# Optimization experiments

Measured on AMD Instinct MI355X. Metric: run time of the kernel, lower is better.

## Reference

```python
import jax, jax.numpy as jnp
import numpy as np

T = 8192  # context/question length (input_shape[2])
D = 128   # feature dim (input_shape[3])


def setup_inputs() -> dict:
    key = jax.random.key(0)
    k1, k2 = jax.random.split(key)
    x = jax.random.normal(k1, (2, 1, T, D), dtype=jnp.float32)
    kernel = jax.random.normal(k2, (3 * D,), dtype=jnp.float32)
    return {"x": x, "kernel": kernel}


def reference(x, kernel):
    context = x[0, 0]   # (T, D)
    question = x[1, 0]  # (T, D)
    w_c, w_q, w_m = kernel[:D], kernel[D:2 * D], kernel[2 * D:]

    # Additive similarity: S[i,j] = c_i.w_c + q_j.w_q + (c_i*q_j).w_m
    # Avoids materializing the (T, T, 3D) tiled/concatenated tensor.
    S = (context @ w_c)[:, None] + (question @ w_q)[None, :] \
        + (context * w_m) @ question.T  # (T, T)

    A = jax.nn.softmax(S, axis=-1)  # row-wise softmax, as tf.nn.softmax on 2D

    # C2Q attention: U_A[i] = sum_j A[i,j] * q_j
    U_A = A @ question  # (T, D)

    # Q2C attention: b = row-max of A, h = sum_i b_i * c_i, tiled over rows
    b = jnp.max(A, axis=1)          # (T,)
    h = b @ context                 # (D,)
    H_A = jnp.broadcast_to(h, (T, D))

    # megamerge: [c, U_A, c*U_A, c*H_A]
    G = jnp.concatenate([context, U_A, context * U_A, context * H_A], axis=-1)
    return G  # (T, 4D)
```

## Files before the change

kernel.cpp:

```cpp
#include <hip/hip_runtime.h>
#include <hip/hip_bf16.h>

#define T 8192
#define D 128
#define NSPLIT 8
#define JLEN (T / NSPLIT)
#define BN 64
#define NITER (JLEN / BN)
#define BM 128
#define LOG2E 1.44269504088896f

typedef _Float16 half2_t __attribute__((ext_vector_type(2)));
typedef _Float16 half4_t __attribute__((ext_vector_type(4)));
typedef _Float16 half8_t __attribute__((ext_vector_type(8)));
typedef __fp16 fp16x2_t __attribute__((ext_vector_type(2)));
typedef float floatx4 __attribute__((ext_vector_type(4)));
typedef float floatx16 __attribute__((ext_vector_type(16)));

__global__ void prep_kernel(const float* __restrict__ x, const float* __restrict__ kern,
                            _Float16* __restrict__ q16, _Float16* __restrict__ qT16,
                            _Float16* __restrict__ cm16, float* __restrict__ qq2) {
    const float* context  = x;
    const float* question = x + (size_t)T * D;
    const float* wq = kern + D;
    const float* wm = kern + 2 * D;
    __shared__ __align__(16) _Float16 tile[32][136];
    int j0 = blockIdx.x * 32;
    int t = threadIdx.x;
    int c4 = t & 31;
    int rsub = t >> 5;
    float4 wqv = ((const float4*)wq)[c4];
    float4 wmv = ((const float4*)wm)[c4];
    for (int p = 0; p < 4; ++p) {
        int row = p * 8 + rsub;
        float4 q = ((const float4*)(question + (size_t)(j0 + row) * D))[c4];
        float4 c = ((const float4*)(context  + (size_t)(j0 + row) * D))[c4];
        half4_t qh;
        qh[0] = (_Float16)q.x; qh[1] = (_Float16)q.y; qh[2] = (_Float16)q.z; qh[3] = (_Float16)q.w;
        *(half4_t*)(q16 + (size_t)(j0 + row) * D + c4 * 4) = qh;
        *(half4_t*)&tile[row][c4 * 4] = qh;
        half4_t ch;
        ch[0] = (_Float16)(c.x * wmv.x * LOG2E); ch[1] = (_Float16)(c.y * wmv.y * LOG2E);
        ch[2] = (_Float16)(c.z * wmv.z * LOG2E); ch[3] = (_Float16)(c.w * wmv.w * LOG2E);
        *(half4_t*)(cm16 + (size_t)(j0 + row) * D + c4 * 4) = ch;
        float s = q.x * wqv.x + q.y * wqv.y + q.z * wqv.z + q.w * wqv.w;
        for (int dx = 1; dx <= 16; dx <<= 1) s += __shfl_xor(s, dx);
        if (c4 == 0) qq2[j0 + row] = s * LOG2E;
    }
    __syncthreads();
    for (int p = 0; p < 2; ++p) {
        int chunk = t + p * 256;
        int d = chunk >> 2, jo = (chunk & 3) * 8;
        half8_t v;
        for (int s2 = 0; s2 < 8; ++s2) v[s2] = tile[jo + s2][d];
        *(half8_t*)(qT16 + (size_t)d * T + j0 + jo) = v;
    }
}

__global__ __launch_bounds__(256, 2)
void flash_kernel(const _Float16* __restrict__ q16, const _Float16* __restrict__ qT16,
                  const _Float16* __restrict__ cm16, const float* __restrict__ qq2,
                  unsigned char* __restrict__ Opart, float* __restrict__ mpart,
                  float* __restrict__ lpart) {
    __shared__ __align__(16) _Float16 Kt[2][64][136];
    __shared__ __align__(16) _Float16 Vt[2][128][64];
    __shared__ __align__(16) float qqs[JLEN];

    const int bx = blockIdx.x;
    const int rb = bx >> 3;
    const int sp = bx & 7;
    const int tid = threadIdx.x;
    const int wave = tid >> 6;
    const int lane = tid & 63;
    const int l31 = lane & 31;
    const int h = lane >> 5;
    const int rbase = rb * BM + wave * 32;
    const int q = rbase + l31;
    const int sig = (l31 & 19) | ((l31 & 4) << 1) | ((l31 & 8) >> 1);

    ((float4*)qqs)[tid] = ((const float4*)(qq2 + (size_t)sp * JLEN))[tid];

    half8_t qfrag[8];
#pragma unroll
    for (int ks = 0; ks < 8; ++ks)
        qfrag[ks] = *(const half8_t*)(cm16 + (size_t)q * D + ks * 16 + h * 8);

    floatx16 acc[4];
#pragma unroll
    for (int nt = 0; nt < 4; ++nt)
#pragma unroll
        for (int r = 0; r < 16; ++r) acc[nt][r] = 0.f;
    float m_run = -INFINITY, l_run = 0.f;

    const int j0 = sp * JLEN;
    half8_t kreg[4], vreg[4];
#pragma unroll
    for (int k = 0; k < 4; ++k) {
        int idx = tid + k * 256;
        kreg[k] = *(const half8_t*)(q16 + (size_t)(j0 + (idx >> 4)) * D + (idx & 15) * 8);
        vreg[k] = *(const half8_t*)(qT16 + (size_t)(idx >> 3) * T + j0 + (idx & 7) * 8);
    }
#pragma unroll
    for (int k = 0; k < 4; ++k) {
        int idx = tid + k * 256;
        *(half8_t*)&Kt[0][idx >> 4][(idx & 15) * 8] = kreg[k];
        int dr = idx >> 3, c8 = idx & 7;
        *(half8_t*)&Vt[0][dr][((c8 + (dr & 7)) & 7) * 8] = vreg[k];
    }
#pragma unroll
    for (int k = 0; k < 4; ++k) {
        int idx = tid + k * 256;
        kreg[k] = *(const half8_t*)(q16 + (size_t)(j0 + BN + (idx >> 4)) * D + (idx & 15) * 8);
        vreg[k] = *(const half8_t*)(qT16 + (size_t)(idx >> 3) * T + j0 + BN + (idx & 7) * 8);
    }
    __syncthreads();

    for (int it = 0; it < NITER; ++it) {
        const int cur = it & 1;
        if (it + 1 < NITER) {
#pragma unroll
            for (int k = 0; k < 4; ++k) {
                int idx = tid + k * 256;
                *(half8_t*)&Kt[cur ^ 1][idx >> 4][(idx & 15) * 8] = kreg[k];
                int dr = idx >> 3, c8 = idx & 7;
                *(half8_t*)&Vt[cur ^ 1][dr][((c8 + (dr & 7)) & 7) * 8] = vreg[k];
            }
        }
        if (it + 2 < NITER) {
            int jn = j0 + (it + 2) * BN;
#pragma unroll
            for (int k = 0; k < 4; ++k) {
                int idx = tid + k * 256;
                kreg[k] = *(const half8_t*)(q16 + (size_t)(jn + (idx >> 4)) * D + (idx & 15) * 8);
                vreg[k] = *(const half8_t*)(qT16 + (size_t)(idx >> 3) * T + jn + (idx & 7) * 8);
            }
        }

        floatx16 St[2];
#pragma unroll
        for (int jt = 0; jt < 2; ++jt) {
            const float* qb = &qqs[it * 64 + jt * 32];
            float4 b0 = *(const float4*)(qb + 8 * h);
            float4 b1 = *(const float4*)(qb + 4 + 8 * h);
            float4 b2 = *(const float4*)(qb + 16 + 8 * h);
            float4 b3 = *(const float4*)(qb + 20 + 8 * h);
            St[jt][0]  = b0.x; St[jt][1]  = b0.y; St[jt][2]  = b0.z; St[jt][3]  = b0.w;
            St[jt][4]  = b1.x; St[jt][5]  = b1.y; St[jt][6]  = b1.z; St[jt][7]  = b1.w;
            St[jt][8]  = b2.x; St[jt][9]  = b2.y; St[jt][10] = b2.z; St[jt][11] = b2.w;
            St[jt][12] = b3.x; St[jt][13] = b3.y; St[jt][14] = b3.z; St[jt][15] = b3.w;
            __builtin_amdgcn_s_setprio(1);
#pragma unroll
            for (int ks = 0; ks < 8; ++ks) {
                half8_t a = *(const half8_t*)&Kt[cur][jt * 32 + sig][ks * 16 + h * 8];
                St[jt] = __builtin_amdgcn_mfma_f32_32x32x16_f16(a, qfrag[ks], St[jt], 0, 0, 0);
            }
            __builtin_amdgcn_s_setprio(0);
        }

        float mx = St[0][0];
#pragma unroll
        for (int r = 1; r < 16; ++r) mx = fmaxf(mx, St[0][r]);
#pragma unroll
        for (int r = 0; r < 16; ++r) mx = fmaxf(mx, St[1][r]);
        mx = fmaxf(mx, __shfl_xor(mx, 32));
        if (__any(mx > m_run)) {
            float mnew = fmaxf(m_run, mx);
            float alpha = __builtin_amdgcn_exp2f(m_run - mnew);
#pragma unroll
            for (int nt = 0; nt < 4; ++nt)
#pragma unroll
                for (int r = 0; r < 16; ++r) acc[nt][r] *= alpha;
            l_run *= alpha;
            m_run = mnew;
        }
        half2_t pp[2][8];
        float ps = 0.f;
#pragma unroll
        for (int jt = 0; jt < 2; ++jt)
#pragma unroll
            for (int r2 = 0; r2 < 8; ++r2) {
                float p0 = __builtin_amdgcn_exp2f(St[jt][2 * r2]     - m_run);
                float p1 = __builtin_amdgcn_exp2f(St[jt][2 * r2 + 1] - m_run);
                ps += p0 + p1;
                fp16x2_t pk = __builtin_amdgcn_cvt_pkrtz(p0, p1);
                pp[jt][r2] = __builtin_bit_cast(half2_t, pk);
            }
        ps += __shfl_xor(ps, 32);
        l_run += ps;

        __builtin_amdgcn_s_setprio(1);
#pragma unroll
        for (int jt = 0; jt < 2; ++jt)
#pragma unroll
            for (int kb = 0; kb < 2; ++kb) {
                half8_t pb;
                pb[0] = pp[jt][kb * 4 + 0][0]; pb[1] = pp[jt][kb * 4 + 0][1];
                pb[2] = pp[jt][kb * 4 + 1][0]; pb[3] = pp[jt][kb * 4 + 1][1];
                pb[4] = pp[jt][kb * 4 + 2][0]; pb[5] = pp[jt][kb * 4 + 2][1];
                pb[6] = pp[jt][kb * 4 + 3][0]; pb[7] = pp[jt][kb * 4 + 3][1];
                const int pg = ((jt * 4 + kb * 2 + h) + (l31 & 7)) & 7;
#pragma unroll
                for (int nt = 0; nt < 4; ++nt) {
                    half8_t va = *(const half8_t*)&Vt[cur][nt * 32 + l31][pg * 8];
                    acc[nt] = __builtin_amdgcn_mfma_f32_32x32x16_f16(va, pb, acc[nt], 0, 0, 0);
                }
            }
        __builtin_amdgcn_s_setprio(0);
        __syncthreads();
    }

    if (h == 0) {
        mpart[(size_t)sp * T + q] = m_run;
        lpart[(size_t)sp * T + q] = l_run;
    }
    float rinv = 1.0f / l_run;
#pragma unroll
    for (int nt = 0; nt < 4; ++nt)
#pragma unroll
        for (int rg = 0; rg < 4; ++rg) {
            float v0 = acc[nt][rg * 4 + 0] * rinv;
            float v1 = acc[nt][rg * 4 + 1] * rinv;
            float v2 = acc[nt][rg * 4 + 2] * rinv;
            float v3 = acc[nt][rg * 4 + 3] * rinv;
            unsigned u = (unsigned)__builtin_amdgcn_cvt_pk_fp8_f32(v0, v1, 0, false);
            u = (unsigned)__builtin_amdgcn_cvt_pk_fp8_f32(v2, v3, u, true);
            *(unsigned*)(Opart + ((size_t)sp * T + q) * D + nt * 32 + rg * 8 + 4 * h) = u;
        }
}

__global__ void combine_kernel(const float* __restrict__ x, const float* __restrict__ mpart,
                               const float* __restrict__ lpart, float* __restrict__ hpart) {
    __shared__ float linv_s[128];
    int b = blockIdx.x, t = threadIdx.x;
    if (t < 128) {
        int i = b * 128 + t;
        float mp[NSPLIT];
        float mstar = -INFINITY;
        for (int sp2 = 0; sp2 < NSPLIT; ++sp2) {
            mp[sp2] = mpart[(size_t)sp2 * T + i];
            mstar = fmaxf(mstar, mp[sp2]);
        }
        float L = 0.f;
        for (int sp2 = 0; sp2 < NSPLIT; ++sp2)
            L += __builtin_amdgcn_exp2f(mp[sp2] - mstar) * lpart[(size_t)sp2 * T + i];
        linv_s[t] = 1.0f / L;
    }
    __syncthreads();
    int d = t & 127, g = t >> 7;
    int r0 = g * 64;
    float s = 0.f;
    for (int r = 0; r < 64; ++r)
        s += x[(size_t)(b * 128 + r0 + r) * D + d] * linv_s[r0 + r];
    hpart[(size_t)(b * 2 + g) * 128 + d] = s;
}

__global__ void merge_kernel(const unsigned char* __restrict__ Opart, const float* __restrict__ mpart,
                             const float* __restrict__ lpart, float* __restrict__ U_A,
                             const float* __restrict__ hpart, float* __restrict__ h) {
    int t = threadIdx.x;
    if (blockIdx.x == 0 && t < 128) {
        float s = 0.f;
        for (int k = 0; k < 128; ++k) s += hpart[(size_t)k * 128 + t];
        h[t] = s;
    }
    int i = blockIdx.x * 16 + (t >> 4);
    int c = t & 15;
    float mp[NSPLIT];
    float mstar = -INFINITY;
    for (int sp = 0; sp < NSPLIT; ++sp) {
        mp[sp] = mpart[(size_t)sp * T + i];
        mstar = fmaxf(mstar, mp[sp]);
    }
    float L = 0.f;
    float u[8];
    for (int k = 0; k < 8; ++k) u[k] = 0.f;
    int d0 = c * 8;
    for (int sp = 0; sp < NSPLIT; ++sp) {
        float w = __builtin_amdgcn_exp2f(mp[sp] - mstar) * lpart[(size_t)sp * T + i];
        L += w;
        uint2 ow = *(const uint2*)(Opart + ((size_t)sp * T + i) * D + d0);
        u[0] += __builtin_amdgcn_cvt_f32_fp8(ow.x, 0) * w;
        u[1] += __builtin_amdgcn_cvt_f32_fp8(ow.x, 1) * w;
        u[2] += __builtin_amdgcn_cvt_f32_fp8(ow.x, 2) * w;
        u[3] += __builtin_amdgcn_cvt_f32_fp8(ow.x, 3) * w;
        u[4] += __builtin_amdgcn_cvt_f32_fp8(ow.y, 0) * w;
        u[5] += __builtin_amdgcn_cvt_f32_fp8(ow.y, 1) * w;
        u[6] += __builtin_amdgcn_cvt_f32_fp8(ow.y, 2) * w;
        u[7] += __builtin_amdgcn_cvt_f32_fp8(ow.y, 3) * w;
    }
    float invL = 1.0f / L;
    float4 s0 = make_float4(u[0] * invL, u[1] * invL, u[2] * invL, u[3] * invL);
    float4 s1 = make_float4(u[4] * invL, u[5] * invL, u[6] * invL, u[7] * invL);
    *(float4*)(U_A + (size_t)i * D + d0) = s0;
    *(float4*)(U_A + (size_t)i * D + d0 + 4) = s1;
}

__global__ void assemble_kernel(const float* __restrict__ x, const float* __restrict__ U_A,
                                const float* __restrict__ h, float* __restrict__ out) {
    const float* context = x;
    int gid = blockIdx.x * 256 + threadIdx.x;
    int base = gid * 4;
    int i = base >> 9;
    int c = base & 511;
    int seg = c >> 7, d = c & 127;
    float4 r;
    if (seg == 0) {
        r = *(const float4*)(context + (size_t)i * D + d);
    } else if (seg == 1) {
        r = *(const float4*)(U_A + (size_t)i * D + d);
    } else if (seg == 2) {
        float4 a = *(const float4*)(context + (size_t)i * D + d);
        float4 b = *(const float4*)(U_A + (size_t)i * D + d);
        r = make_float4(a.x * b.x, a.y * b.y, a.z * b.z, a.w * b.w);
    } else {
        float4 a = *(const float4*)(context + (size_t)i * D + d);
        float4 b = *(const float4*)(h + d);
        r = make_float4(a.x * b.x, a.y * b.y, a.z * b.z, a.w * b.w);
    }
    *(float4*)(out + base) = r;
}

extern "C" void kernel_launch(void* const* d_in, const int* in_sizes, int n_in,
                              void* d_out, int out_size, void* d_ws, size_t ws_size,
                              hipStream_t stream) {
    const float* x = (const float*)d_in[0];
    const float* kern = (const float*)d_in[1];
    float* out = (float*)d_out;

    char* w = (char*)d_ws;
    size_t off = 0;
    _Float16* q16  = (_Float16*)(w + off); off += (size_t)T * D * 2;
    _Float16* qT16 = (_Float16*)(w + off); off += (size_t)T * D * 2;
    _Float16* cm16 = (_Float16*)(w + off); off += (size_t)T * D * 2;
    float* qq2   = (float*)(w + off); off += (size_t)T * 4;
    float* mpart = (float*)(w + off); off += (size_t)NSPLIT * T * 4;
    float* lpart = (float*)(w + off); off += (size_t)NSPLIT * T * 4;
    float* U_A   = (float*)(w + off); off += (size_t)T * D * 4;
    float* hpart = (float*)(w + off); off += (size_t)128 * 128 * 4;
    float* h     = (float*)(w + off); off += (size_t)D * 4;

    unsigned char* Opart = (unsigned char*)d_out;

    prep_kernel<<<256, 256, 0, stream>>>(x, kern, q16, qT16, cm16, qq2);
    flash_kernel<<<512, 256, 0, stream>>>(q16, qT16, cm16, qq2, Opart, mpart, lpart);
    combine_kernel<<<64, 256, 0, stream>>>(x, mpart, lpart, hpart);
    merge_kernel<<<512, 256, 0, stream>>>(Opart, mpart, lpart, U_A, hpart, h);
    assemble_kernel<<<4096, 256, 0, stream>>>(x, U_A, h, out);
}
```

Measured before the change: 127.9 us.

## Software-pipeline QK MFMA one tile ahead and fuse combine/merge into one launch

The flash kernel now computes the score tile for the next iteration while running the softmax and PV MMA for the current one. It also splits the K and V shared-memory stores around a mid-loop barrier that replaces the end-of-loop one, and uses tree reductions for the row max and partial sums. The combine and merge kernels become a single tail kernel whose extra blocks accumulate h with atomicAdd, with h zeroed in the prep kernel, which saves one launch and the hpart reduction. The cost is more live registers for the second score tile, which can lower occupancy, and float atomic ordering makes h nondeterministic.

```diff
diff --git a/kernel.cpp b/kernel.cpp
--- a/kernel.cpp
+++ b/kernel.cpp
@@ -19,7 +19,8 @@
 
 __global__ void prep_kernel(const float* __restrict__ x, const float* __restrict__ kern,
                             _Float16* __restrict__ q16, _Float16* __restrict__ qT16,
-                            _Float16* __restrict__ cm16, float* __restrict__ qq2) {
+                            _Float16* __restrict__ cm16, float* __restrict__ qq2,
+                            float* __restrict__ h) {
     const float* context  = x;
     const float* question = x + (size_t)T * D;
     const float* wq = kern + D;
@@ -27,6 +28,7 @@
     __shared__ __align__(16) _Float16 tile[32][136];
     int j0 = blockIdx.x * 32;
     int t = threadIdx.x;
+    if (blockIdx.x == 0 && t < 128) h[t] = 0.f;
     int c4 = t & 31;
     int rsub = t >> 5;
     float4 wqv = ((const float4*)wq)[c4];
@@ -115,6 +117,25 @@
     }
     __syncthreads();
 
+    floatx16 Sp[2];
+#pragma unroll
+    for (int jt = 0; jt < 2; ++jt) {
+        const float* qb = &qqs[jt * 32];
+        float4 b0 = *(const float4*)(qb + 8 * h);
+        float4 b1 = *(const float4*)(qb + 4 + 8 * h);
+        float4 b2 = *(const float4*)(qb + 16 + 8 * h);
+        float4 b3 = *(const float4*)(qb + 20 + 8 * h);
+        Sp[jt][0]  = b0.x; Sp[jt][1]  = b0.y; Sp[jt][2]  = b0.z; Sp[jt][3]  = b0.w;
+        Sp[jt][4]  = b1.x; Sp[jt][5]  = b1.y; Sp[jt][6]  = b1.z; Sp[jt][7]  = b1.w;
+        Sp[jt][8]  = b2.x; Sp[jt][9]  = b2.y; Sp[jt][10] = b2.z; Sp[jt][11] = b2.w;
+        Sp[jt][12] = b3.x; Sp[jt][13] = b3.y; Sp[jt][14] = b3.z; Sp[jt][15] = b3.w;
+#pragma unroll
+        for (int ks = 0; ks < 8; ++ks) {
+            half8_t a = *(const half8_t*)&Kt[0][jt * 32 + sig][ks * 16 + h * 8];
+            Sp[jt] = __builtin_amdgcn_mfma_f32_32x32x16_f16(a, qfrag[ks], Sp[jt], 0, 0, 0);
+        }
+    }
+
     for (int it = 0; it < NITER; ++it) {
         const int cur = it & 1;
         if (it + 1 < NITER) {
@@ -122,6 +143,13 @@
             for (int k = 0; k < 4; ++k) {
                 int idx = tid + k * 256;
                 *(half8_t*)&Kt[cur ^ 1][idx >> 4][(idx & 15) * 8] = kreg[k];
+            }
+        }
+        __syncthreads();
+        if (it + 1 < NITER) {
+#pragma unroll
+            for (int k = 0; k < 4; ++k) {
+                int idx = tid + k * 256;
                 int dr = idx >> 3, c8 = idx & 7;
                 *(half8_t*)&Vt[cur ^ 1][dr][((c8 + (dr & 7)) & 7) * 8] = vreg[k];
             }
@@ -136,32 +164,35 @@
             }
         }
 
-        floatx16 St[2];
-#pragma unroll
-        for (int jt = 0; jt < 2; ++jt) {
-            const float* qb = &qqs[it * 64 + jt * 32];
-            float4 b0 = *(const float4*)(qb + 8 * h);
-            float4 b1 = *(const float4*)(qb + 4 + 8 * h);
-            float4 b2 = *(const float4*)(qb + 16 + 8 * h);
-            float4 b3 = *(const float4*)(qb + 20 + 8 * h);
-            St[jt][0]  = b0.x; St[jt][1]  = b0.y; St[jt][2]  = b0.z; St[jt][3]  = b0.w;
-            St[jt][4]  = b1.x; St[jt][5]  = b1.y; St[jt][6]  = b1.z; St[jt][7]  = b1.w;
-            St[jt][8]  = b2.x; St[jt][9]  = b2.y; St[jt][10] = b2.z; St[jt][11] = b2.w;
-            St[jt][12] = b3.x; St[jt][13] = b3.y; St[jt][14] = b3.z; St[jt][15] = b3.w;
-            __builtin_amdgcn_s_setprio(1);
-#pragma unroll
-            for (int ks = 0; ks < 8; ++ks) {
-                half8_t a = *(const half8_t*)&Kt[cur][jt * 32 + sig][ks * 16 + h * 8];
-                St[jt] = __builtin_amdgcn_mfma_f32_32x32x16_f16(a, qfrag[ks], St[jt], 0, 0, 0);
-            }
-            __builtin_amdgcn_s_setprio(0);
-        }
-
-        float mx = St[0][0];
-#pragma unroll
-        for (int r = 1; r < 16; ++r) mx = fmaxf(mx, St[0][r]);
-#pragma unroll
-        for (int r = 0; r < 16; ++r) mx = fmaxf(mx, St[1][r]);
+        floatx16 Sn[2];
+        if (it + 1 < NITER) {
+#pragma unroll
+            for (int jt = 0; jt < 2; ++jt) {
+                const float* qb = &qqs[(it + 1) * 64 + jt * 32];
+                float4 b0 = *(const float4*)(qb + 8 * h);
+                float4 b1 = *(const float4*)(qb + 4 + 8 * h);
+                float4 b2 = *(const float4*)(qb + 16 + 8 * h);
+                float4 b3 = *(const float4*)(qb + 20 + 8 * h);
+                Sn[jt][0]  = b0.x; Sn[jt][1]  = b0.y; Sn[jt][2]  = b0.z; Sn[jt][3]  = b0.w;
+                Sn[jt][4]  = b1.x; Sn[jt][5]  = b1.y; Sn[jt][6]  = b1.z; Sn[jt][7]  = b1.w;
+                Sn[jt][8]  = b2.x; Sn[jt][9]  = b2.y; Sn[jt][10] = b2.z; Sn[jt][11] = b2.w;
+                Sn[jt][12] = b3.x; Sn[jt][13] = b3.y; Sn[jt][14] = b3.z; Sn[jt][15] = b3.w;
+                __builtin_amdgcn_s_setprio(1);
+#pragma unroll
+                for (int ks = 0; ks < 8; ++ks) {
+                    half8_t a = *(const half8_t*)&Kt[cur ^ 1][jt * 32 + sig][ks * 16 + h * 8];
+                    Sn[jt] = __builtin_amdgcn_mfma_f32_32x32x16_f16(a, qfrag[ks], Sn[jt], 0, 0, 0);
+                }
+                __builtin_amdgcn_s_setprio(0);
+            }
+        }
+
+        float t8[8];
+#pragma unroll
+        for (int r = 0; r < 8; ++r)
+            t8[r] = fmaxf(fmaxf(Sp[0][r], Sp[0][r + 8]), fmaxf(Sp[1][r], Sp[1][r + 8]));
+        float mx = fmaxf(fmaxf(fmaxf(t8[0], t8[4]), fmaxf(t8[1], t8[5])),
+                         fmaxf(fmaxf(t8[2], t8[6]), fmaxf(t8[3], t8[7])));
         mx = fmaxf(mx, __shfl_xor(mx, 32));
         if (__any(mx > m_run)) {
             float mnew = fmaxf(m_run, mx);
@@ -173,18 +204,21 @@
             l_run *= alpha;
             m_run = mnew;
         }
-        half2_t pp[2][8];
-        float ps = 0.f;
+        int pk_[2][2][4];
+        float psa[4] = {0.f, 0.f, 0.f, 0.f};
 #pragma unroll
         for (int jt = 0; jt < 2; ++jt)
 #pragma unroll
-            for (int r2 = 0; r2 < 8; ++r2) {
-                float p0 = __builtin_amdgcn_exp2f(St[jt][2 * r2]     - m_run);
-                float p1 = __builtin_amdgcn_exp2f(St[jt][2 * r2 + 1] - m_run);
-                ps += p0 + p1;
-                fp16x2_t pk = __builtin_amdgcn_cvt_pkrtz(p0, p1);
-                pp[jt][r2] = __builtin_bit_cast(half2_t, pk);
-            }
+            for (int kb = 0; kb < 2; ++kb)
+#pragma unroll
+                for (int r = 0; r < 4; ++r) {
+                    float p0 = __builtin_amdgcn_exp2f(Sp[jt][kb * 8 + 2 * r]     - m_run);
+                    float p1 = __builtin_amdgcn_exp2f(Sp[jt][kb * 8 + 2 * r + 1] - m_run);
+                    psa[r] += p0 + p1;
+                    fp16x2_t pk = __builtin_amdgcn_cvt_pkrtz(p0, p1);
+                    pk_[jt][kb][r] = __builtin_bit_cast(int, pk);
+                }
+        float ps = (psa[0] + psa[1]) + (psa[2] + psa[3]);
         ps += __shfl_xor(ps, 32);
         l_run += ps;
 
@@ -193,11 +227,10 @@
         for (int jt = 0; jt < 2; ++jt)
 #pragma unroll
             for (int kb = 0; kb < 2; ++kb) {
-                half8_t pb;
-                pb[0] = pp[jt][kb * 4 + 0][0]; pb[1] = pp[jt][kb * 4 + 0][1];
-                pb[2] = pp[jt][kb * 4 + 1][0]; pb[3] = pp[jt][kb * 4 + 1][1];
-                pb[4] = pp[jt][kb * 4 + 2][0]; pb[5] = pp[jt][kb * 4 + 2][1];
-                pb[6] = pp[jt][kb * 4 + 3][0]; pb[7] = pp[jt][kb * 4 + 3][1];
+                int4 w;
+                w.x = pk_[jt][kb][0]; w.y = pk_[jt][kb][1];
+                w.z = pk_[jt][kb][2]; w.w = pk_[jt][kb][3];
+                half8_t pb = __builtin_bit_cast(half8_t, w);
                 const int pg = ((jt * 4 + kb * 2 + h) + (l31 & 7)) & 7;
 #pragma unroll
                 for (int nt = 0; nt < 4; ++nt) {
@@ -206,7 +239,8 @@
                 }
             }
         __builtin_amdgcn_s_setprio(0);
-        __syncthreads();
+
+        if (it + 1 < NITER) { Sp[0] = Sn[0]; Sp[1] = Sn[1]; }
     }
 
     if (h == 0) {
@@ -228,40 +262,34 @@
         }
 }
 
-__global__ void combine_kernel(const float* __restrict__ x, const float* __restrict__ mpart,
-                               const float* __restrict__ lpart, float* __restrict__ hpart) {
+__global__ void tail_kernel(const unsigned char* __restrict__ Opart, const float* __restrict__ mpart,
+                            const float* __restrict__ lpart, const float* __restrict__ x,
+                            float* __restrict__ U_A, float* __restrict__ h) {
     __shared__ float linv_s[128];
-    int b = blockIdx.x, t = threadIdx.x;
-    if (t < 128) {
-        int i = b * 128 + t;
-        float mp[NSPLIT];
-        float mstar = -INFINITY;
-        for (int sp2 = 0; sp2 < NSPLIT; ++sp2) {
-            mp[sp2] = mpart[(size_t)sp2 * T + i];
-            mstar = fmaxf(mstar, mp[sp2]);
-        }
-        float L = 0.f;
-        for (int sp2 = 0; sp2 < NSPLIT; ++sp2)
-            L += __builtin_amdgcn_exp2f(mp[sp2] - mstar) * lpart[(size_t)sp2 * T + i];
-        linv_s[t] = 1.0f / L;
-    }
-    __syncthreads();
-    int d = t & 127, g = t >> 7;
-    int r0 = g * 64;
-    float s = 0.f;
-    for (int r = 0; r < 64; ++r)
-        s += x[(size_t)(b * 128 + r0 + r) * D + d] * linv_s[r0 + r];
-    hpart[(size_t)(b * 2 + g) * 128 + d] = s;
-}
-
-__global__ void merge_kernel(const unsigned char* __restrict__ Opart, const float* __restrict__ mpart,
-                             const float* __restrict__ lpart, float* __restrict__ U_A,
-                             const float* __restrict__ hpart, float* __restrict__ h) {
     int t = threadIdx.x;
-    if (blockIdx.x == 0 && t < 128) {
+    if (blockIdx.x >= 512) {
+        int b = blockIdx.x - 512;
+        if (t < 128) {
+            int i = b * 128 + t;
+            float mp[NSPLIT];
+            float mstar = -INFINITY;
+            for (int sp2 = 0; sp2 < NSPLIT; ++sp2) {
+                mp[sp2] = mpart[(size_t)sp2 * T + i];
+                mstar = fmaxf(mstar, mp[sp2]);
+            }
+            float L = 0.f;
+            for (int sp2 = 0; sp2 < NSPLIT; ++sp2)
+                L += __builtin_amdgcn_exp2f(mp[sp2] - mstar) * lpart[(size_t)sp2 * T + i];
+            linv_s[t] = 1.0f / L;
+        }
+        __syncthreads();
+        int d = t & 127, g = t >> 7;
+        int r0 = g * 64;
         float s = 0.f;
-        for (int k = 0; k < 128; ++k) s += hpart[(size_t)k * 128 + t];
-        h[t] = s;
+        for (int r = 0; r < 64; ++r)
+            s += x[(size_t)(b * 128 + r0 + r) * D + d] * linv_s[r0 + r];
+        atomicAdd(&h[d], s);
+        return;
     }
     int i = blockIdx.x * 16 + (t >> 4);
     int c = t & 15;
@@ -336,14 +364,12 @@
     float* mpart = (float*)(w + off); off += (size_t)NSPLIT * T * 4;
     float* lpart = (float*)(w + off); off += (size_t)NSPLIT * T * 4;
     float* U_A   = (float*)(w + off); off += (size_t)T * D * 4;
-    float* hpart = (float*)(w + off); off += (size_t)128 * 128 * 4;
     float* h     = (float*)(w + off); off += (size_t)D * 4;
 
     unsigned char* Opart = (unsigned char*)d_out;
 
-    prep_kernel<<<256, 256, 0, stream>>>(x, kern, q16, qT16, cm16, qq2);
+    prep_kernel<<<256, 256, 0, stream>>>(x, kern, q16, qT16, cm16, qq2, h);
     flash_kernel<<<512, 256, 0, stream>>>(q16, qT16, cm16, qq2, Opart, mpart, lpart);
-    combine_kernel<<<64, 256, 0, stream>>>(x, mpart, lpart, hpart);
-    merge_kernel<<<512, 256, 0, stream>>>(Opart, mpart, lpart, U_A, hpart, h);
+    tail_kernel<<<576, 256, 0, stream>>>(Opart, mpart, lpart, x, U_A, h);
     assemble_kernel<<<4096, 256, 0, stream>>>(x, U_A, h, out);
 }
```

Result: slower. 150.4 us (+17.6%).

## Fuse combine and merge into one tail kernel with atomic h reduction; pad Vt LDS

Applied to the files above, without the earlier changes.

Removes the separate combine kernel by computing the row-max-weighted context sum inside the merge kernel. It uses the already-computed 1/L, wave shuffles, an LDS reduction and atomicAdd into h, which prep_kernel now zeroes. This saves one kernel launch and the extra reads of mpart, lpart and x. Separately, the Vt shared-memory tile row is padded from 64 to 72 halves to reduce LDS bank conflicts. The atomics make the h summation order nondeterministic, and the padding raises LDS usage, which may affect occupancy.

```diff
diff --git a/kernel.cpp b/kernel.cpp
--- a/kernel.cpp
+++ b/kernel.cpp
@@ -19,7 +19,8 @@
 
 __global__ void prep_kernel(const float* __restrict__ x, const float* __restrict__ kern,
                             _Float16* __restrict__ q16, _Float16* __restrict__ qT16,
-                            _Float16* __restrict__ cm16, float* __restrict__ qq2) {
+                            _Float16* __restrict__ cm16, float* __restrict__ qq2,
+                            float* __restrict__ h) {
     const float* context  = x;
     const float* question = x + (size_t)T * D;
     const float* wq = kern + D;
@@ -27,6 +28,7 @@
     __shared__ __align__(16) _Float16 tile[32][136];
     int j0 = blockIdx.x * 32;
     int t = threadIdx.x;
+    if (blockIdx.x == 0 && t < 128) h[t] = 0.f;
     int c4 = t & 31;
     int rsub = t >> 5;
     float4 wqv = ((const float4*)wq)[c4];
@@ -63,7 +65,7 @@
                   unsigned char* __restrict__ Opart, float* __restrict__ mpart,
                   float* __restrict__ lpart) {
     __shared__ __align__(16) _Float16 Kt[2][64][136];
-    __shared__ __align__(16) _Float16 Vt[2][128][64];
+    __shared__ __align__(16) _Float16 Vt[2][128][72];
     __shared__ __align__(16) float qqs[JLEN];
 
     const int bx = blockIdx.x;
@@ -228,41 +230,11 @@
         }
 }
 
-__global__ void combine_kernel(const float* __restrict__ x, const float* __restrict__ mpart,
-                               const float* __restrict__ lpart, float* __restrict__ hpart) {
-    __shared__ float linv_s[128];
-    int b = blockIdx.x, t = threadIdx.x;
-    if (t < 128) {
-        int i = b * 128 + t;
-        float mp[NSPLIT];
-        float mstar = -INFINITY;
-        for (int sp2 = 0; sp2 < NSPLIT; ++sp2) {
-            mp[sp2] = mpart[(size_t)sp2 * T + i];
-            mstar = fmaxf(mstar, mp[sp2]);
-        }
-        float L = 0.f;
-        for (int sp2 = 0; sp2 < NSPLIT; ++sp2)
-            L += __builtin_amdgcn_exp2f(mp[sp2] - mstar) * lpart[(size_t)sp2 * T + i];
-        linv_s[t] = 1.0f / L;
-    }
-    __syncthreads();
-    int d = t & 127, g = t >> 7;
-    int r0 = g * 64;
-    float s = 0.f;
-    for (int r = 0; r < 64; ++r)
-        s += x[(size_t)(b * 128 + r0 + r) * D + d] * linv_s[r0 + r];
-    hpart[(size_t)(b * 2 + g) * 128 + d] = s;
-}
-
-__global__ void merge_kernel(const unsigned char* __restrict__ Opart, const float* __restrict__ mpart,
-                             const float* __restrict__ lpart, float* __restrict__ U_A,
-                             const float* __restrict__ hpart, float* __restrict__ h) {
+__global__ void tail_kernel(const unsigned char* __restrict__ Opart, const float* __restrict__ mpart,
+                            const float* __restrict__ lpart, const float* __restrict__ x,
+                            float* __restrict__ U_A, float* __restrict__ h) {
+    __shared__ float wsum[4][128];
     int t = threadIdx.x;
-    if (blockIdx.x == 0 && t < 128) {
-        float s = 0.f;
-        for (int k = 0; k < 128; ++k) s += hpart[(size_t)k * 128 + t];
-        h[t] = s;
-    }
     int i = blockIdx.x * 16 + (t >> 4);
     int c = t & 15;
     float mp[NSPLIT];
@@ -293,6 +265,24 @@
     float4 s1 = make_float4(u[4] * invL, u[5] * invL, u[6] * invL, u[7] * invL);
     *(float4*)(U_A + (size_t)i * D + d0) = s0;
     *(float4*)(U_A + (size_t)i * D + d0 + 4) = s1;
+
+    float4 ca = *(const float4*)(x + (size_t)i * D + d0);
+    float4 cb = *(const float4*)(x + (size_t)i * D + d0 + 4);
+    float hv[8] = { ca.x * invL, ca.y * invL, ca.z * invL, ca.w * invL,
+                    cb.x * invL, cb.y * invL, cb.z * invL, cb.w * invL };
+#pragma unroll
+    for (int k = 0; k < 8; ++k) {
+        hv[k] += __shfl_xor(hv[k], 16);
+        hv[k] += __shfl_xor(hv[k], 32);
+    }
+    int lane = t & 63, wv = t >> 6;
+    if (lane < 16) {
+#pragma unroll
+        for (int k = 0; k < 8; ++k) wsum[wv][lane * 8 + k] = hv[k];
+    }
+    __syncthreads();
+    if (t < 128)
+        atomicAdd(&h[t], (wsum[0][t] + wsum[1][t]) + (wsum[2][t] + wsum[3][t]));
 }
 
 __global__ void assemble_kernel(const float* __restrict__ x, const float* __restrict__ U_A,
@@ -336,14 +326,12 @@
     float* mpart = (float*)(w + off); off += (size_t)NSPLIT * T * 4;
     float* lpart = (float*)(w + off); off += (size_t)NSPLIT * T * 4;
     float* U_A   = (float*)(w + off); off += (size_t)T * D * 4;
-    float* hpart = (float*)(w + off); off += (size_t)128 * 128 * 4;
     float* h     = (float*)(w + off); off += (size_t)D * 4;
 
     unsigned char* Opart = (unsigned char*)d_out;
 
-    prep_kernel<<<256, 256, 0, stream>>>(x, kern, q16, qT16, cm16, qq2);
+    prep_kernel<<<256, 256, 0, stream>>>(x, kern, q16, qT16, cm16, qq2, h);
     flash_kernel<<<512, 256, 0, stream>>>(q16, qT16, cm16, qq2, Opart, mpart, lpart);
-    combine_kernel<<<64, 256, 0, stream>>>(x, mpart, lpart, hpart);
-    merge_kernel<<<512, 256, 0, stream>>>(Opart, mpart, lpart, U_A, hpart, h);
+    tail_kernel<<<512, 256, 0, stream>>>(Opart, mpart, lpart, x, U_A, h);
     assemble_kernel<<<4096, 256, 0, stream>>>(x, U_A, h, out);
 }
```

Result: slower. 134.0 us (+4.7%).

## Software-pipeline PV MFMA one step behind QK and store V/P in FP8

Applied to the files above, without the earlier changes.

The flash loop now issues the P·V MFMAs for the previous tile after the Q·K MFMAs of the current tile, so the softmax exp work can overlap with matrix-core work. To support this, V tiles use a three-slot LDS ring and P fragments alternate between two register sets. The loop is manually unrolled by two and a tail step handles the last tile. V is converted to FP8 when staged into LDS and P is packed to FP8, so P·V runs on fp8 MFMAs. That halves LDS footprint and traffic for V, but adds conversion instructions and loses accuracy in the attention weights and values.

```diff
diff --git a/kernel.cpp b/kernel.cpp
--- a/kernel.cpp
+++ b/kernel.cpp
@@ -63,15 +63,15 @@
                   unsigned char* __restrict__ Opart, float* __restrict__ mpart,
                   float* __restrict__ lpart) {
     __shared__ __align__(16) _Float16 Kt[2][64][136];
-    __shared__ __align__(16) _Float16 Vt[2][128][64];
+    __shared__ __align__(16) unsigned char Vt8[3][128 * 72];
     __shared__ __align__(16) float qqs[JLEN];
 
     const int bx = blockIdx.x;
     const int rb = bx >> 3;
     const int sp = bx & 7;
     const int tid = threadIdx.x;
+    const int lane = tid & 63;
     const int wave = tid >> 6;
-    const int lane = tid & 63;
     const int l31 = lane & 31;
     const int h = lane >> 5;
     const int rbase = rb * BM + wave * 32;
@@ -94,6 +94,10 @@
 
     const int j0 = sp * JLEN;
     half8_t kreg[4], vreg[4];
+    long ppE[4], ppO[4];
+#pragma unroll
+    for (int k = 0; k < 4; ++k) { ppE[k] = 0; ppO[k] = 0; }
+
 #pragma unroll
     for (int k = 0; k < 4; ++k) {
         int idx = tid + k * 256;
@@ -104,8 +108,12 @@
     for (int k = 0; k < 4; ++k) {
         int idx = tid + k * 256;
         *(half8_t*)&Kt[0][idx >> 4][(idx & 15) * 8] = kreg[k];
-        int dr = idx >> 3, c8 = idx & 7;
-        *(half8_t*)&Vt[0][dr][((c8 + (dr & 7)) & 7) * 8] = vreg[k];
+        int drr = idx >> 3, g = idx & 7;
+        unsigned u0 = (unsigned)__builtin_amdgcn_cvt_pk_fp8_f32((float)vreg[k][0], (float)vreg[k][1], 0, false);
+        u0 = (unsigned)__builtin_amdgcn_cvt_pk_fp8_f32((float)vreg[k][2], (float)vreg[k][3], u0, true);
+        unsigned u1 = (unsigned)__builtin_amdgcn_cvt_pk_fp8_f32((float)vreg[k][4], (float)vreg[k][5], 0, false);
+        u1 = (unsigned)__builtin_amdgcn_cvt_pk_fp8_f32((float)vreg[k][6], (float)vreg[k][7], u1, true);
+        *(uint2*)&Vt8[0][drr * 72 + ((g + (drr & 7)) & 7) * 8] = make_uint2(u0, u1);
     }
 #pragma unroll
     for (int k = 0; k < 4; ++k) {
@@ -115,99 +123,145 @@
     }
     __syncthreads();
 
-    for (int it = 0; it < NITER; ++it) {
-        const int cur = it & 1;
-        if (it + 1 < NITER) {
-#pragma unroll
-            for (int k = 0; k < 4; ++k) {
-                int idx = tid + k * 256;
-                *(half8_t*)&Kt[cur ^ 1][idx >> 4][(idx & 15) * 8] = kreg[k];
-                int dr = idx >> 3, c8 = idx & 7;
-                *(half8_t*)&Vt[cur ^ 1][dr][((c8 + (dr & 7)) & 7) * 8] = vreg[k];
+#define FBODY(IT, PPW, PPR)                                                          \
+    do {                                                                             \
+        const int cur = (IT) & 1;                                                    \
+        const int vsw = ((IT) + 1) % 3;                                              \
+        const int vsr = ((IT) + 2) % 3;                                              \
+        if ((IT) + 1 < NITER) {                                                      \
+            _Pragma("unroll")                                                        \
+            for (int k = 0; k < 4; ++k) {                                            \
+                int idx = tid + k * 256;                                             \
+                *(half8_t*)&Kt[cur ^ 1][idx >> 4][(idx & 15) * 8] = kreg[k];         \
+            }                                                                        \
+            _Pragma("unroll")                                                        \
+            for (int k = 0; k < 4; ++k) {                                            \
+                int idx = tid + k * 256;                                             \
+                int drr = idx >> 3, g = idx & 7;                                     \
+                unsigned u0 = (unsigned)__builtin_amdgcn_cvt_pk_fp8_f32(             \
+                    (float)vreg[k][0], (float)vreg[k][1], 0, false);                 \
+                u0 = (unsigned)__builtin_amdgcn_cvt_pk_fp8_f32(                      \
+                    (float)vreg[k][2], (float)vreg[k][3], u0, true);                 \
+                unsigned u1 = (unsigned)__builtin_amdgcn_cvt_pk_fp8_f32(             \
+                    (float)vreg[k][4], (float)vreg[k][5], 0, false);                 \
+                u1 = (unsigned)__builtin_amdgcn_cvt_pk_fp8_f32(                      \
+                    (float)vreg[k][6], (float)vreg[k][7], u1, true);                 \
+                *(uint2*)&Vt8[vsw][drr * 72 + ((g + (drr & 7)) & 7) * 8] =           \
+                    make_uint2(u0, u1);                                              \
+            }                                                                        \
+        }                                                                            \
+        if ((IT) + 2 < NITER) {                                                      \
+            int jn = j0 + ((IT) + 2) * BN;                                           \
+            _Pragma("unroll")                                                        \
+            for (int k = 0; k < 4; ++k) {                                            \
+                int idx = tid + k * 256;                                             \
+                kreg[k] = *(const half8_t*)(q16 + (size_t)(jn + (idx >> 4)) * D      \
+                                            + (idx & 15) * 8);                       \
+                vreg[k] = *(const half8_t*)(qT16 + (size_t)(idx >> 3) * T + jn       \
+                                            + (idx & 7) * 8);                        \
+            }                                                                        \
+        }                                                                            \
+        floatx16 St[2];                                                              \
+        _Pragma("unroll")                                                            \
+        for (int jt = 0; jt < 2; ++jt) {                                             \
+            const float* qb = &qqs[(IT) * 64 + jt * 32];                             \
+            float4 b0 = *(const float4*)(qb + 8 * h);                                \
+            float4 b1 = *(const float4*)(qb + 4 + 8 * h);                            \
+            float4 b2 = *(const float4*)(qb + 16 + 8 * h);                           \
+            float4 b3 = *(const float4*)(qb + 20 + 8 * h);                           \
+            St[jt][0] = b0.x; St[jt][1] = b0.y; St[jt][2] = b0.z; St[jt][3] = b0.w;  \
+            St[jt][4] = b1.x; St[jt][5] = b1.y; St[jt][6] = b1.z; St[jt][7] = b1.w;  \
+            St[jt][8] = b2.x; St[jt][9] = b2.y; St[jt][10] = b2.z; St[jt][11] = b2.w;\
+            St[jt][12] = b3.x; St[jt][13] = b3.y; St[jt][14] = b3.z; St[jt][15] = b3.w;\
+            __builtin_amdgcn_s_setprio(1);                                           \
+            _Pragma("unroll")                                                        \
+            for (int ks = 0; ks < 8; ++ks) {                                         \
+                half8_t a = *(const half8_t*)&Kt[cur][jt * 32 + sig][ks * 16 + h * 8];\
+                St[jt] = __builtin_amdgcn_mfma_f32_32x32x16_f16(a, qfrag[ks],        \
+                                                                St[jt], 0, 0, 0);    \
+            }                                                                        \
+            __builtin_amdgcn_s_setprio(0);                                           \
+        }                                                                            \
+        if ((IT) > 0) {                                                              \
+            __builtin_amdgcn_s_setprio(1);                                           \
+            _Pragma("unroll")                                                        \
+            for (int jt = 0; jt < 2; ++jt)                                           \
+                _Pragma("unroll")                                                    \
+                for (int kb = 0; kb < 2; ++kb) {                                     \
+                    long pb = PPR[jt * 2 + kb];                                      \
+                    _Pragma("unroll")                                                \
+                    for (int nt = 0; nt < 4; ++nt) {                                 \
+                        int row = nt * 32 + l31;                                     \
+                        int pg = ((jt * 4 + kb * 2 + h) + (row & 7)) & 7;            \
+                        long va = *(const long*)&Vt8[vsr][row * 72 + pg * 8];        \
+                        acc[nt] = __builtin_amdgcn_mfma_f32_32x32x16_fp8_fp8(        \
+                            va, pb, acc[nt], 0, 0, 0);                               \
+                    }                                                                \
+                }                                                                    \
+            __builtin_amdgcn_s_setprio(0);                                           \
+        }                                                                            \
+        float mx = St[0][0];                                                         \
+        _Pragma("unroll")                                                            \
+        for (int r = 1; r < 16; ++r) mx = fmaxf(mx, St[0][r]);                       \
+        _Pragma("unroll")                                                            \
+        for (int r = 0; r < 16; ++r) mx = fmaxf(mx, St[1][r]);                       \
+        mx = fmaxf(mx, __shfl_xor(mx, 32));                                          \
+        if (__any(mx > m_run)) {                                                     \
+            float mnew = fmaxf(m_run, mx);                                           \
+            float alpha = __builtin_amdgcn_exp2f(m_run - mnew);                      \
+            _Pragma("unroll")                                                        \
+            for (int nt = 0; nt < 4; ++nt)                                           \
+                _Pragma("unroll")                                                    \
+                for (int r = 0; r < 16; ++r) acc[nt][r] *= alpha;                    \
+            l_run *= alpha;                                                          \
+            m_run = mnew;                                                            \
+        }                                                                            \
+        float ps = 0.f;                                                              \
+        _Pragma("unroll")                                                            \
+        for (int jt = 0; jt < 2; ++jt)                                               \
+            _Pragma("unroll")                                                        \
+            for (int kb = 0; kb < 2; ++kb) {                                         \
+                float p0 = __builtin_amdgcn_exp2f(St[jt][kb * 8 + 0] - m_run);       \
+                float p1 = __builtin_amdgcn_exp2f(St[jt][kb * 8 + 1] - m_run);       \
+                float p2 = __builtin_amdgcn_exp2f(St[jt][kb * 8 + 2] - m_run);       \
+                float p3 = __builtin_amdgcn_exp2f(St[jt][kb * 8 + 3] - m_run);       \
+                float p4 = __builtin_amdgcn_exp2f(St[jt][kb * 8 + 4] - m_run);       \
+                float p5 = __builtin_amdgcn_exp2f(St[jt][kb * 8 + 5] - m_run);       \
+                float p6 = __builtin_amdgcn_exp2f(St[jt][kb * 8 + 6] - m_run);       \
+                float p7 = __builtin_amdgcn_exp2f(St[jt][kb * 8 + 7] - m_run);       \
+                ps += ((p0 + p1) + (p2 + p3)) + ((p4 + p5) + (p6 + p7));             \
+                unsigned a0 = (unsigned)__builtin_amdgcn_cvt_pk_fp8_f32(p0, p1, 0, false);\
+                a0 = (unsigned)__builtin_amdgcn_cvt_pk_fp8_f32(p2, p3, a0, true);    \
+                unsigned a1 = (unsigned)__builtin_amdgcn_cvt_pk_fp8_f32(p4, p5, 0, false);\
+                a1 = (unsigned)__builtin_amdgcn_cvt_pk_fp8_f32(p6, p7, a1, true);    \
+                PPW[jt * 2 + kb] = (long)(((unsigned long long)a1 << 32) | a0);      \
+            }                                                                        \
+        ps += __shfl_xor(ps, 32);                                                    \
+        l_run += ps;                                                                 \
+        __syncthreads();                                                             \
+    } while (0)
+
+    for (int it2 = 0; it2 < NITER; it2 += 2) {
+        FBODY(it2, ppE, ppO);
+        FBODY(it2 + 1, ppO, ppE);
+    }
+#undef FBODY
+
+    __builtin_amdgcn_s_setprio(1);
+#pragma unroll
+    for (int jt = 0; jt < 2; ++jt)
+#pragma unroll
+        for (int kb = 0; kb < 2; ++kb) {
+            long pb = ppO[jt * 2 + kb];
+#pragma unroll
+            for (int nt = 0; nt < 4; ++nt) {
+                int row = nt * 32 + l31;
+                int pg = ((jt * 4 + kb * 2 + h) + (row & 7)) & 7;
+                long va = *(const long*)&Vt8[(NITER - 1) % 3][row * 72 + pg * 8];
+                acc[nt] = __builtin_amdgcn_mfma_f32_32x32x16_fp8_fp8(va, pb, acc[nt], 0, 0, 0);
             }
         }
-        if (it + 2 < NITER) {
-            int jn = j0 + (it + 2) * BN;
-#pragma unroll
-            for (int k = 0; k < 4; ++k) {
-                int idx = tid + k * 256;
-                kreg[k] = *(const half8_t*)(q16 + (size_t)(jn + (idx >> 4)) * D + (idx & 15) * 8);
-                vreg[k] = *(const half8_t*)(qT16 + (size_t)(idx >> 3) * T + jn + (idx & 7) * 8);
-            }
-        }
-
-        floatx16 St[2];
-#pragma unroll
-        for (int jt = 0; jt < 2; ++jt) {
-            const float* qb = &qqs[it * 64 + jt * 32];
-            float4 b0 = *(const float4*)(qb + 8 * h);
-            float4 b1 = *(const float4*)(qb + 4 + 8 * h);
-            float4 b2 = *(const float4*)(qb + 16 + 8 * h);
-            float4 b3 = *(const float4*)(qb + 20 + 8 * h);
-            St[jt][0]  = b0.x; St[jt][1]  = b0.y; St[jt][2]  = b0.z; St[jt][3]  = b0.w;
-            St[jt][4]  = b1.x; St[jt][5]  = b1.y; St[jt][6]  = b1.z; St[jt][7]  = b1.w;
-            St[jt][8]  = b2.x; St[jt][9]  = b2.y; St[jt][10] = b2.z; St[jt][11] = b2.w;
-            St[jt][12] = b3.x; St[jt][13] = b3.y; St[jt][14] = b3.z; St[jt][15] = b3.w;
-            __builtin_amdgcn_s_setprio(1);
-#pragma unroll
-            for (int ks = 0; ks < 8; ++ks) {
-                half8_t a = *(const half8_t*)&Kt[cur][jt * 32 + sig][ks * 16 + h * 8];
-                St[jt] = __builtin_amdgcn_mfma_f32_32x32x16_f16(a, qfrag[ks], St[jt], 0, 0, 0);
-            }
-            __builtin_amdgcn_s_setprio(0);
-        }
-
-        float mx = St[0][0];
-#pragma unroll
-        for (int r = 1; r < 16; ++r) mx = fmaxf(mx, St[0][r]);
-#pragma unroll
-        for (int r = 0; r < 16; ++r) mx = fmaxf(mx, St[1][r]);
-        mx = fmaxf(mx, __shfl_xor(mx, 32));
-        if (__any(mx > m_run)) {
-            float mnew = fmaxf(m_run, mx);
-            float alpha = __builtin_amdgcn_exp2f(m_run - mnew);
-#pragma unroll
-            for (int nt = 0; nt < 4; ++nt)
-#pragma unroll
-                for (int r = 0; r < 16; ++r) acc[nt][r] *= alpha;
-            l_run *= alpha;
-            m_run = mnew;
-        }
-        half2_t pp[2][8];
-        float ps = 0.f;
-#pragma unroll
-        for (int jt = 0; jt < 2; ++jt)
-#pragma unroll
-            for (int r2 = 0; r2 < 8; ++r2) {
-                float p0 = __builtin_amdgcn_exp2f(St[jt][2 * r2]     - m_run);
-                float p1 = __builtin_amdgcn_exp2f(St[jt][2 * r2 + 1] - m_run);
-                ps += p0 + p1;
-                fp16x2_t pk = __builtin_amdgcn_cvt_pkrtz(p0, p1);
-                pp[jt][r2] = __builtin_bit_cast(half2_t, pk);
-            }
-        ps += __shfl_xor(ps, 32);
-        l_run += ps;
-
-        __builtin_amdgcn_s_setprio(1);
-#pragma unroll
-        for (int jt = 0; jt < 2; ++jt)
-#pragma unroll
-            for (int kb = 0; kb < 2; ++kb) {
-                half8_t pb;
-                pb[0] = pp[jt][kb * 4 + 0][0]; pb[1] = pp[jt][kb * 4 + 0][1];
-                pb[2] = pp[jt][kb * 4 + 1][0]; pb[3] = pp[jt][kb * 4 + 1][1];
-                pb[4] = pp[jt][kb * 4 + 2][0]; pb[5] = pp[jt][kb * 4 + 2][1];
-                pb[6] = pp[jt][kb * 4 + 3][0]; pb[7] = pp[jt][kb * 4 + 3][1];
-                const int pg = ((jt * 4 + kb * 2 + h) + (l31 & 7)) & 7;
-#pragma unroll
-                for (int nt = 0; nt < 4; ++nt) {
-                    half8_t va = *(const half8_t*)&Vt[cur][nt * 32 + l31][pg * 8];
-                    acc[nt] = __builtin_amdgcn_mfma_f32_32x32x16_f16(va, pb, acc[nt], 0, 0, 0);
-                }
-            }
-        __builtin_amdgcn_s_setprio(0);
-        __syncthreads();
-    }
+    __builtin_amdgcn_s_setprio(0);
 
     if (h == 0) {
         mpart[(size_t)sp * T + q] = m_run;
```

Result: no change. 128.4 us (+0.4%).
